# Kernel tuning notes

Hardware: AMD Instinct MI355X
Metric: run time of the kernel (lower is better)

Reference implementation:

```python
import jax, jax.numpy as jnp
import numpy as np

T, K, E, H, I = 2048, 8, 32, 1024, 768


def setup_inputs() -> dict:
    key = jax.random.key(0)
    k0, k1, k2, k3, k4, k5 = jax.random.split(key, 6)
    sh = 1.0 / np.sqrt(H).astype(np.float32)
    si = 1.0 / np.sqrt(I).astype(np.float32)
    return {
        "hidden_states": jax.random.normal(k0, (T, H), jnp.float32),
        "top_k_index": jax.random.randint(k1, (T, K), 0, E),
        "top_k_weights": jax.random.uniform(k2, (T, K), jnp.float32),
        "gate_proj": jax.random.normal(k3, (E, I, H), jnp.float32) * sh,
        "up_proj": jax.random.normal(k4, (E, I, H), jnp.float32) * sh,
        "down_proj": jax.random.normal(k5, (E, H, I), jnp.float32) * si,
    }


def reference(hidden_states, top_k_index, top_k_weights, gate_proj, up_proj, down_proj):
    # Tokens not routed to expert e get combine weight 0, so summing the
    # weighted per-expert outputs over all experts reproduces the original
    # gather -> SwiGLU MLP -> scale -> index_add_ exactly (duplicated expert
    # hits within a token's top-k sum, matching repeated index_add_).
    n_tok = hidden_states.shape[0]
    n_exp = gate_proj.shape[0]
    combine = jnp.zeros((n_tok, n_exp), hidden_states.dtype)
    combine = combine.at[jnp.arange(n_tok)[:, None], top_k_index].add(top_k_weights)

    def body(acc, xs):
        g_w, u_w, d_w, w_e = xs  # g_w,u_w: [I,H]; d_w: [H,I]; w_e: [T]
        h = jax.nn.silu(hidden_states @ g_w.T) * (hidden_states @ u_w.T)  # [T,I]
        y = h @ d_w.T  # [T,H]
        return acc + y * w_e[:, None], None

    out, _ = jax.lax.scan(
        body,
        jnp.zeros_like(hidden_states),
        (gate_proj, up_proj, down_proj, combine.T),
    )
    return out
```

## Files before the change

### kernel.cpp

```cpp
#include <hip/hip_runtime.h>

#define T_TOK 2048
#define TOPK  8
#define NEXP  32
#define HDIM  1024
#define IDIM  768
#define NPAIR (T_TOK * TOPK)
#define BM 128
#define BK 32
#define MT_MAX (NPAIR / BM + NEXP)

typedef __attribute__((ext_vector_type(8))) short short8;
typedef __attribute__((ext_vector_type(4))) float f32x4;

__device__ __forceinline__ unsigned short f2bf(float f) {
    unsigned x = __float_as_uint(f);
    unsigned r = x + 0x7fffu + ((x >> 16) & 1u);
    return (unsigned short)(r >> 16);
}
__device__ __forceinline__ float bf2f(unsigned short u) {
    return __uint_as_float(((unsigned)u) << 16);
}

__device__ __forceinline__ void gl_lds16(const unsigned short* g, void* l) {
    __builtin_amdgcn_global_load_lds((const __attribute__((address_space(1))) void*)g,
                                     (__attribute__((address_space(3))) void*)l, 16, 0, 0);
}

__device__ __forceinline__ int mt_swz(int bx) {
    return ((bx >> 4) << 4) | ((bx & 7) << 1) | ((bx >> 3) & 1);
}

#define WSYNC do { \
    asm volatile("s_waitcnt vmcnt(0)" ::: "memory"); \
    __builtin_amdgcn_s_barrier(); \
    __builtin_amdgcn_sched_barrier(0); \
} while (0)

__global__ void k_conv2(const float* __restrict__ src0, const float* __restrict__ src1,
                        unsigned short* __restrict__ dst, int n4each) {
    int i = blockIdx.x * 256 + threadIdx.x;
    const float* s = (i < n4each) ? src0 : src1;
    int j = (i < n4each) ? i : i - n4each;
    if (i < 2 * n4each) {
        float4 v = ((const float4*)s)[j];
        ushort4 o;
        o.x = f2bf(v.x); o.y = f2bf(v.y); o.z = f2bf(v.z); o.w = f2bf(v.w);
        ((ushort4*)dst)[i] = o;
    }
}

__global__ void k_conv(const float* __restrict__ src, unsigned short* __restrict__ dst, int n4) {
    int i = blockIdx.x * 256 + threadIdx.x;
    if (i < n4) {
        float4 v = ((const float4*)src)[i];
        ushort4 o;
        o.x = f2bf(v.x); o.y = f2bf(v.y); o.z = f2bf(v.z); o.w = f2bf(v.w);
        ((ushort4*)dst)[i] = o;
    }
}

__global__ void k_init(int* counts) {
    if (threadIdx.x < NEXP) counts[threadIdx.x] = 0;
}

__global__ void k_hist(const int* __restrict__ idx, int* __restrict__ counts) {
    int p = blockIdx.x * 256 + threadIdx.x;
    atomicAdd(&counts[idx[p]], 1);
}

__global__ void k_scan(const int* __restrict__ counts, int* __restrict__ offsets,
                       int* __restrict__ mtb, int* __restrict__ cursor) {
    if (threadIdx.x == 0) {
        int tot = 0, mt = 0;
        for (int e = 0; e < NEXP; ++e) {
            offsets[e] = tot; mtb[e] = mt;
            tot += counts[e];
            mt += (counts[e] + BM - 1) / BM;
        }
        offsets[NEXP] = tot; mtb[NEXP] = mt;
    }
    if (threadIdx.x < NEXP) cursor[threadIdx.x] = 0;
}

__global__ void k_scatter(const int* __restrict__ idx, int* __restrict__ cursor,
                          const int* __restrict__ offsets, int* __restrict__ pair_token,
                          int* __restrict__ pair_slot) {
    int p = blockIdx.x * 256 + threadIdx.x;
    int e = idx[p];
    int pos = atomicAdd(&cursor[e], 1);
    int slot = offsets[e] + pos;
    pair_token[slot] = p >> 3;
    pair_slot[p] = slot;
}

__global__ __launch_bounds__(256, 2) void k_gateup(
    const unsigned short* __restrict__ hid_bf, const unsigned short* __restrict__ gate_bf,
    const unsigned short* __restrict__ up_bf, const int* __restrict__ pair_token,
    const int* __restrict__ offsets, const int* __restrict__ mtb,
    unsigned short* __restrict__ h_mid)
{
    __shared__ short8 sBuf[2][1536];
    __shared__ int sInfo[4];
    int tid = threadIdx.x;
    int mt = mt_swz(blockIdx.x);
    if (tid == 0 && mt >= mtb[NEXP]) sInfo[0] = -1;
    if (tid < NEXP) {
        int lo = mtb[tid], hi = mtb[tid + 1];
        if (lo <= mt && mt < hi) {
            sInfo[0] = tid; sInfo[1] = offsets[tid];
            sInfo[2] = offsets[tid + 1] - offsets[tid];
            sInfo[3] = (mt - lo) * BM;
        }
    }
    __syncthreads();
    int e = sInfo[0];
    if (e < 0) return;
    int off = sInfo[1], Me = sInfo[2], mrow0 = sInfo[3];
    int n0 = blockIdx.y * 128;

    int wave = tid >> 6, lane = tid & 63, quad = lane >> 4, l16 = lane & 15;

    int m0 = wave * 32 + l16, m1 = m0 + 16;
    int rp0 = mrow0 + m0, rp1 = mrow0 + m1;
    int tok0 = (rp0 < Me) ? pair_token[off + rp0] : 0;
    int tok1 = (rp1 < Me) ? pair_token[off + rp1] : 0;
    const unsigned short* aG0 = hid_bf + (size_t)tok0 * HDIM + quad * 8;
    const unsigned short* aG1 = hid_bf + (size_t)tok1 * HDIM + quad * 8;
    const unsigned short* gG0 = gate_bf + ((size_t)e * IDIM + n0 + m0) * HDIM + quad * 8;
    const unsigned short* gG1 = gate_bf + ((size_t)e * IDIM + n0 + m1) * HDIM + quad * 8;
    const unsigned short* uG0 = up_bf + ((size_t)e * IDIM + n0 + m0) * HDIM + quad * 8;
    const unsigned short* uG1 = up_bf + ((size_t)e * IDIM + n0 + m1) * HDIM + quad * 8;
    const int dA = wave * 128;
    const int dG = 512 + wave * 128;
    const int dU = 1024 + wave * 128;

    int wm = (wave & 1) * 64, wn = (wave >> 1) * 64;
    int aBase = (wm >> 4) * 64 + quad * 16 + l16;
    int bBase = (wn >> 4) * 64 + quad * 16 + l16;

    f32x4 zero = {0.f, 0.f, 0.f, 0.f};
    f32x4 accg[4][4], accu[4][4];
#pragma unroll
    for (int i = 0; i < 4; ++i)
#pragma unroll
        for (int j = 0; j < 4; ++j) { accg[i][j] = zero; accu[i][j] = zero; }

#define STAGE_GU(b, k0) do { \
        short8* nb_ = &sBuf[b][0]; \
        gl_lds16(aG0 + (k0), (void*)(nb_ + dA));      gl_lds16(aG1 + (k0), (void*)(nb_ + dA + 64)); \
        gl_lds16(gG0 + (k0), (void*)(nb_ + dG));      gl_lds16(gG1 + (k0), (void*)(nb_ + dG + 64)); \
        gl_lds16(uG0 + (k0), (void*)(nb_ + dU));      gl_lds16(uG1 + (k0), (void*)(nb_ + dU + 64)); \
    } while (0)

#define COMP_GU(b) do { \
        const short8* cb_ = &sBuf[b][0]; \
        short8 af_[4]; \
        _Pragma("unroll") for (int fm = 0; fm < 4; ++fm) af_[fm] = cb_[aBase + fm * 64]; \
        _Pragma("unroll") for (int fn = 0; fn < 4; ++fn) { \
            short8 bg_ = cb_[512 + bBase + fn * 64]; \
            short8 bu_ = cb_[1024 + bBase + fn * 64]; \
            _Pragma("unroll") for (int fm = 0; fm < 4; ++fm) { \
                accg[fm][fn] = __builtin_amdgcn_mfma_f32_16x16x32_bf16(af_[fm], bg_, accg[fm][fn], 0, 0, 0); \
                accu[fm][fn] = __builtin_amdgcn_mfma_f32_16x16x32_bf16(af_[fm], bu_, accu[fm][fn], 0, 0, 0); \
            } \
        } \
    } while (0)

    STAGE_GU(0, 0);
    WSYNC;
#pragma unroll 1
    for (int it = 0; it < HDIM / BK; it += 2) {
        STAGE_GU(1, (it + 1) * BK);
        COMP_GU(0);
        WSYNC;
        if (it + 2 < HDIM / BK) STAGE_GU(0, (it + 2) * BK);
        COMP_GU(1);
        WSYNC;
    }

#pragma unroll
    for (int fm = 0; fm < 4; ++fm)
#pragma unroll
        for (int fn = 0; fn < 4; ++fn)
#pragma unroll
            for (int r = 0; r < 4; ++r) {
                int mloc = wm + fm * 16 + quad * 4 + r;
                int prow = mrow0 + mloc;
                if (prow < Me) {
                    int col = n0 + wn + fn * 16 + l16;
                    float g = accg[fm][fn][r], u = accu[fm][fn][r];
                    float h = g / (1.f + __expf(-g)) * u;
                    h_mid[(size_t)(off + prow) * IDIM + col] = f2bf(h);
                }
            }
}

__global__ __launch_bounds__(256, 2) void k_down(
    const unsigned short* __restrict__ h_mid, const unsigned short* __restrict__ down_bf,
    const int* __restrict__ offsets, const int* __restrict__ mtb,
    unsigned short* __restrict__ y_pair)
{
    __shared__ short8 sBuf[2][1536];
    __shared__ int sInfo[4];
    int tid = threadIdx.x;
    int mt = mt_swz(blockIdx.x);
    if (tid == 0 && mt >= mtb[NEXP]) sInfo[0] = -1;
    if (tid < NEXP) {
        int lo = mtb[tid], hi = mtb[tid + 1];
        if (lo <= mt && mt < hi) {
            sInfo[0] = tid; sInfo[1] = offsets[tid];
            sInfo[2] = offsets[tid + 1] - offsets[tid];
            sInfo[3] = (mt - lo) * BM;
        }
    }
    __syncthreads();
    int e = sInfo[0];
    if (e < 0) return;
    int off = sInfo[1], Me = sInfo[2], mrow0 = sInfo[3];
    int n0 = blockIdx.y * 256;

    int wave = tid >> 6, lane = tid & 63, quad = lane >> 4, l16 = lane & 15;

    int m0 = wave * 32 + l16, m1 = m0 + 16;
    int rp0 = mrow0 + m0; if (rp0 >= Me) rp0 = 0;
    int rp1 = mrow0 + m1; if (rp1 >= Me) rp1 = 0;
    const unsigned short* aG0 = h_mid + (size_t)(off + rp0) * IDIM + quad * 8;
    const unsigned short* aG1 = h_mid + (size_t)(off + rp1) * IDIM + quad * 8;
    const unsigned short* bG0 = down_bf + ((size_t)e * HDIM + n0 + wave * 64 + l16) * IDIM + quad * 8;
    const unsigned short* bG1 = bG0 + (size_t)16 * IDIM;
    const unsigned short* bG2 = bG0 + (size_t)32 * IDIM;
    const unsigned short* bG3 = bG0 + (size_t)48 * IDIM;
    const int dA = wave * 128;
    const int dB = 512 + wave * 256;

    int wm = (wave & 1) * 64, wn = (wave >> 1) * 128;
    int aBase = (wm >> 4) * 64 + quad * 16 + l16;
    int bBase = (wn >> 4) * 64 + quad * 16 + l16;

    f32x4 zero = {0.f, 0.f, 0.f, 0.f};
    f32x4 acc[4][8];
#pragma unroll
    for (int i = 0; i < 4; ++i)
#pragma unroll
        for (int j = 0; j < 8; ++j) acc[i][j] = zero;

#define STAGE_DN(b, k0) do { \
        short8* nb_ = &sBuf[b][0]; \
        gl_lds16(aG0 + (k0), (void*)(nb_ + dA));       gl_lds16(aG1 + (k0), (void*)(nb_ + dA + 64)); \
        gl_lds16(bG0 + (k0), (void*)(nb_ + dB));       gl_lds16(bG1 + (k0), (void*)(nb_ + dB + 64)); \
        gl_lds16(bG2 + (k0), (void*)(nb_ + dB + 128)); gl_lds16(bG3 + (k0), (void*)(nb_ + dB + 192)); \
    } while (0)

#define COMP_DN(b) do { \
        const short8* cb_ = &sBuf[b][0]; \
        short8 af_[4]; \
        _Pragma("unroll") for (int fm = 0; fm < 4; ++fm) af_[fm] = cb_[aBase + fm * 64]; \
        _Pragma("unroll") for (int fn = 0; fn < 8; ++fn) { \
            short8 bb_ = cb_[512 + bBase + fn * 64]; \
            _Pragma("unroll") for (int fm = 0; fm < 4; ++fm) \
                acc[fm][fn] = __builtin_amdgcn_mfma_f32_16x16x32_bf16(af_[fm], bb_, acc[fm][fn], 0, 0, 0); \
        } \
    } while (0)

    STAGE_DN(0, 0);
    WSYNC;
#pragma unroll 1
    for (int it = 0; it < IDIM / BK; it += 2) {
        STAGE_DN(1, (it + 1) * BK);
        COMP_DN(0);
        WSYNC;
        if (it + 2 < IDIM / BK) STAGE_DN(0, (it + 2) * BK);
        COMP_DN(1);
        WSYNC;
    }

#pragma unroll
    for (int fm = 0; fm < 4; ++fm)
#pragma unroll
        for (int fn = 0; fn < 8; ++fn)
#pragma unroll
            for (int r = 0; r < 4; ++r) {
                int mloc = wm + fm * 16 + quad * 4 + r;
                int prow = mrow0 + mloc;
                if (prow < Me) {
                    int col = n0 + wn + fn * 16 + l16;
                    y_pair[(size_t)(off + prow) * HDIM + col] = f2bf(acc[fm][fn][r]);
                }
            }
}

__global__ void k_reduce(const unsigned short* __restrict__ y_pair,
                         const int* __restrict__ pair_slot,
                         const float* __restrict__ topw, float* __restrict__ out)
{
    int t = blockIdx.x;
    __shared__ int ss[TOPK];
    __shared__ float sw[TOPK];
    if (threadIdx.x < TOPK) {
        ss[threadIdx.x] = pair_slot[t * TOPK + threadIdx.x];
        sw[threadIdx.x] = topw[t * TOPK + threadIdx.x];
    }
    __syncthreads();
    int c = threadIdx.x * 4;
    float a0 = 0.f, a1 = 0.f, a2 = 0.f, a3 = 0.f;
    for (int k = 0; k < TOPK; ++k) {
        const unsigned short* yr = y_pair + (size_t)ss[k] * HDIM + c;
        uint2 v = *(const uint2*)yr;
        float w = sw[k];
        a0 += w * bf2f((unsigned short)(v.x & 0xffff));
        a1 += w * bf2f((unsigned short)(v.x >> 16));
        a2 += w * bf2f((unsigned short)(v.y & 0xffff));
        a3 += w * bf2f((unsigned short)(v.y >> 16));
    }
    float4 o = {a0, a1, a2, a3};
    *(float4*)(out + (size_t)t * HDIM + c) = o;
}

extern "C" void kernel_launch(void* const* d_in, const int* in_sizes, int n_in,
                              void* d_out, int out_size, void* d_ws, size_t ws_size,
                              hipStream_t stream) {
    (void)in_sizes; (void)n_in; (void)out_size; (void)ws_size;
    const float* hidden = (const float*)d_in[0];
    const int*   tki    = (const int*)d_in[1];
    const float* tkw    = (const float*)d_in[2];
    const float* gate   = (const float*)d_in[3];
    const float* up     = (const float*)d_in[4];
    const float* down   = (const float*)d_in[5];
    float* out = (float*)d_out;

    char* w = (char*)d_ws;
    unsigned short* h_mid   = (unsigned short*)w;
    unsigned short* hid_bf  = (unsigned short*)(w + 25165824);
    unsigned short* gate_bf = (unsigned short*)(w + 29360128);
    unsigned short* up_bf   = (unsigned short*)(w + 79691776);
    unsigned short* down_bf = gate_bf;
    unsigned short* y_pair  = up_bf;
    int* ib = (int*)(w + 130023424);
    int* pair_token = ib;
    int* pair_slot  = ib + NPAIR;
    int* counts     = ib + 2 * NPAIR;
    int* cursor     = counts + NEXP;
    int* offsets    = cursor + NEXP;
    int* mtb        = offsets + NEXP + 1;

    const int W4 = NEXP * IDIM * HDIM / 4;
    const int H4 = T_TOK * HDIM / 4;

    k_init<<<1, 64, 0, stream>>>(counts);
    k_hist<<<NPAIR / 256, 256, 0, stream>>>(tki, counts);
    k_scan<<<1, 64, 0, stream>>>(counts, offsets, mtb, cursor);
    k_scatter<<<NPAIR / 256, 256, 0, stream>>>(tki, cursor, offsets, pair_token, pair_slot);

    k_conv<<<(H4 + 255) / 256, 256, 0, stream>>>(hidden, hid_bf, H4);
    k_conv2<<<(2 * W4 + 255) / 256, 256, 0, stream>>>(gate, up, gate_bf, W4);

    k_gateup<<<dim3(MT_MAX, IDIM / 128), 256, 0, stream>>>(hid_bf, gate_bf, up_bf,
                                                           pair_token, offsets, mtb, h_mid);

    k_conv<<<(W4 + 255) / 256, 256, 0, stream>>>(down, down_bf, W4);

    k_down<<<dim3(MT_MAX, HDIM / 256), 256, 0, stream>>>(h_mid, down_bf, offsets, mtb, y_pair);
    k_reduce<<<T_TOK, 256, 0, stream>>>(y_pair, pair_slot, tkw, out);
}
```

Before: 560.8 us.

## Keep two K-tiles in flight with partial vmcnt waits in MoE GEMMs

Restructures the double-buffered K loops of the gate/up and down GEMM kernels so that two stages of global-to-LDS loads are issued ahead. Each compute step now waits only on the older stage via vmcnt(6) instead of draining all outstanding loads, with barriers around each compute. The aim is to hide global load latency behind MFMA work rather than stalling on every tile. The risk is that the vmcnt(6) count must exactly match the number of loads per stage, and dropping the sched_barrier lets the compiler reorder around the LDS reads.

```diff
diff --git a/kernel.cpp b/kernel.cpp
--- a/kernel.cpp
+++ b/kernel.cpp
@@ -31,11 +31,8 @@
     return ((bx >> 4) << 4) | ((bx & 7) << 1) | ((bx >> 3) & 1);
 }
 
-#define WSYNC do { \
-    asm volatile("s_waitcnt vmcnt(0)" ::: "memory"); \
-    __builtin_amdgcn_s_barrier(); \
-    __builtin_amdgcn_sched_barrier(0); \
-} while (0)
+#define VMCNT(n) asm volatile("s_waitcnt vmcnt(" #n ")" ::: "memory")
+#define BARRIER  __builtin_amdgcn_s_barrier()
 
 __global__ void k_conv2(const float* __restrict__ src0, const float* __restrict__ src1,
                         unsigned short* __restrict__ dst, int n4each) {
@@ -168,16 +165,14 @@
     } while (0)
 
     STAGE_GU(0, 0);
-    WSYNC;
+    STAGE_GU(1, BK);
 #pragma unroll 1
-    for (int it = 0; it < HDIM / BK; it += 2) {
-        STAGE_GU(1, (it + 1) * BK);
-        COMP_GU(0);
-        WSYNC;
-        if (it + 2 < HDIM / BK) STAGE_GU(0, (it + 2) * BK);
-        COMP_GU(1);
-        WSYNC;
-    }
+    for (int tt = 0; tt < HDIM / BK - 2; tt += 2) {
+        VMCNT(6); BARRIER; COMP_GU(0); BARRIER; STAGE_GU(0, (tt + 2) * BK);
+        VMCNT(6); BARRIER; COMP_GU(1); BARRIER; STAGE_GU(1, (tt + 3) * BK);
+    }
+    VMCNT(6); BARRIER; COMP_GU(0);
+    VMCNT(0); BARRIER; COMP_GU(1);
 
 #pragma unroll
     for (int fm = 0; fm < 4; ++fm)
@@ -264,16 +259,14 @@
     } while (0)
 
     STAGE_DN(0, 0);
-    WSYNC;
+    STAGE_DN(1, BK);
 #pragma unroll 1
-    for (int it = 0; it < IDIM / BK; it += 2) {
-        STAGE_DN(1, (it + 1) * BK);
-        COMP_DN(0);
-        WSYNC;
-        if (it + 2 < IDIM / BK) STAGE_DN(0, (it + 2) * BK);
-        COMP_DN(1);
-        WSYNC;
-    }
+    for (int tt = 0; tt < IDIM / BK - 2; tt += 2) {
+        VMCNT(6); BARRIER; COMP_DN(0); BARRIER; STAGE_DN(0, (tt + 2) * BK);
+        VMCNT(6); BARRIER; COMP_DN(1); BARRIER; STAGE_DN(1, (tt + 3) * BK);
+    }
+    VMCNT(6); BARRIER; COMP_DN(0);
+    VMCNT(0); BARRIER; COMP_DN(1);
 
 #pragma unroll
     for (int fm = 0; fm < 4; ++fm)
```

Measured after the change: 545.5 us. -2.7%, faster.

## Fuse fp32-to-bf16 weight conversion into grouped GEMM load pipeline

Applied to the files above, without the earlier changes.

Drops the separate conversion kernels for the gate, up and down weights. The GEMM kernels now load the fp32 weights straight into registers, convert them to bf16 and write them to LDS, while activations still arrive through direct global-to-LDS loads. The pipeline is rebuilt with explicit vmcnt/lgkmcnt waits so the register prefetch of the next tile overlaps with MFMA compute. This removes a full pass that wrote and re-read about 150MB of weights. In exchange each weight tile is read as fp32 (twice the bytes) and reloaded by every token tile of an expert, with conversion and more VGPR pressure on the critical path.

```diff
diff --git a/kernel.cpp b/kernel.cpp
--- a/kernel.cpp
+++ b/kernel.cpp
@@ -22,6 +22,15 @@
     return __uint_as_float(((unsigned)u) << 16);
 }
 
+__device__ __forceinline__ short8 pack8(float4 a, float4 b) {
+    short8 r;
+    r[0] = (short)f2bf(a.x); r[1] = (short)f2bf(a.y);
+    r[2] = (short)f2bf(a.z); r[3] = (short)f2bf(a.w);
+    r[4] = (short)f2bf(b.x); r[5] = (short)f2bf(b.y);
+    r[6] = (short)f2bf(b.z); r[7] = (short)f2bf(b.w);
+    return r;
+}
+
 __device__ __forceinline__ void gl_lds16(const unsigned short* g, void* l) {
     __builtin_amdgcn_global_load_lds((const __attribute__((address_space(1))) void*)g,
                                      (__attribute__((address_space(3))) void*)l, 16, 0, 0);
@@ -31,24 +40,10 @@
     return ((bx >> 4) << 4) | ((bx & 7) << 1) | ((bx >> 3) & 1);
 }
 
-#define WSYNC do { \
-    asm volatile("s_waitcnt vmcnt(0)" ::: "memory"); \
-    __builtin_amdgcn_s_barrier(); \
-    __builtin_amdgcn_sched_barrier(0); \
-} while (0)
-
-__global__ void k_conv2(const float* __restrict__ src0, const float* __restrict__ src1,
-                        unsigned short* __restrict__ dst, int n4each) {
-    int i = blockIdx.x * 256 + threadIdx.x;
-    const float* s = (i < n4each) ? src0 : src1;
-    int j = (i < n4each) ? i : i - n4each;
-    if (i < 2 * n4each) {
-        float4 v = ((const float4*)s)[j];
-        ushort4 o;
-        o.x = f2bf(v.x); o.y = f2bf(v.y); o.z = f2bf(v.z); o.w = f2bf(v.w);
-        ((ushort4*)dst)[i] = o;
-    }
-}
+#define VMCNT(n)  asm volatile("s_waitcnt vmcnt(" #n ")" ::: "memory")
+#define LGKM0     asm volatile("s_waitcnt lgkmcnt(0)" ::: "memory")
+#define MEMFENCE  asm volatile("" ::: "memory")
+#define BARRIER   __builtin_amdgcn_s_barrier()
 
 __global__ void k_conv(const float* __restrict__ src, unsigned short* __restrict__ dst, int n4) {
     int i = blockIdx.x * 256 + threadIdx.x;
@@ -95,8 +90,8 @@
 }
 
 __global__ __launch_bounds__(256, 2) void k_gateup(
-    const unsigned short* __restrict__ hid_bf, const unsigned short* __restrict__ gate_bf,
-    const unsigned short* __restrict__ up_bf, const int* __restrict__ pair_token,
+    const unsigned short* __restrict__ hid_bf, const float* __restrict__ gateF,
+    const float* __restrict__ upF, const int* __restrict__ pair_token,
     const int* __restrict__ offsets, const int* __restrict__ mtb,
     unsigned short* __restrict__ h_mid)
 {
@@ -127,13 +122,14 @@
     int tok1 = (rp1 < Me) ? pair_token[off + rp1] : 0;
     const unsigned short* aG0 = hid_bf + (size_t)tok0 * HDIM + quad * 8;
     const unsigned short* aG1 = hid_bf + (size_t)tok1 * HDIM + quad * 8;
-    const unsigned short* gG0 = gate_bf + ((size_t)e * IDIM + n0 + m0) * HDIM + quad * 8;
-    const unsigned short* gG1 = gate_bf + ((size_t)e * IDIM + n0 + m1) * HDIM + quad * 8;
-    const unsigned short* uG0 = up_bf + ((size_t)e * IDIM + n0 + m0) * HDIM + quad * 8;
-    const unsigned short* uG1 = up_bf + ((size_t)e * IDIM + n0 + m1) * HDIM + quad * 8;
     const int dA = wave * 128;
-    const int dG = 512 + wave * 128;
-    const int dU = 1024 + wave * 128;
+
+    const float* gF0 = gateF + ((size_t)e * IDIM + n0 + m0) * HDIM + quad * 8;
+    const float* gF1 = gateF + ((size_t)e * IDIM + n0 + m1) * HDIM + quad * 8;
+    const float* uF0 = upF   + ((size_t)e * IDIM + n0 + m0) * HDIM + quad * 8;
+    const float* uF1 = upF   + ((size_t)e * IDIM + n0 + m1) * HDIM + quad * 8;
+    const int wslot0 = wave * 128 + quad * 16 + l16;
+    const int wslot1 = wslot0 + 64;
 
     int wm = (wave & 1) * 64, wn = (wave >> 1) * 64;
     int aBase = (wm >> 4) * 64 + quad * 16 + l16;
@@ -146,11 +142,25 @@
 #pragma unroll
         for (int j = 0; j < 4; ++j) { accg[i][j] = zero; accu[i][j] = zero; }
 
-#define STAGE_GU(b, k0) do { \
-        short8* nb_ = &sBuf[b][0]; \
-        gl_lds16(aG0 + (k0), (void*)(nb_ + dA));      gl_lds16(aG1 + (k0), (void*)(nb_ + dA + 64)); \
-        gl_lds16(gG0 + (k0), (void*)(nb_ + dG));      gl_lds16(gG1 + (k0), (void*)(nb_ + dG + 64)); \
-        gl_lds16(uG0 + (k0), (void*)(nb_ + dU));      gl_lds16(uG1 + (k0), (void*)(nb_ + dU + 64)); \
+    float4 vg0a, vg0b, vg1a, vg1b, vu0a, vu0b, vu1a, vu1b;
+
+#define ADMA_GU(b, kk) do { \
+        gl_lds16(aG0 + (kk), (void*)(&sBuf[b][dA])); \
+        gl_lds16(aG1 + (kk), (void*)(&sBuf[b][dA + 64])); \
+    } while (0)
+
+#define BLOAD_GU(kk) do { \
+        vg0a = *(const float4*)(gF0 + (kk)); vg0b = *(const float4*)(gF0 + (kk) + 4); \
+        vg1a = *(const float4*)(gF1 + (kk)); vg1b = *(const float4*)(gF1 + (kk) + 4); \
+        vu0a = *(const float4*)(uF0 + (kk)); vu0b = *(const float4*)(uF0 + (kk) + 4); \
+        vu1a = *(const float4*)(uF1 + (kk)); vu1b = *(const float4*)(uF1 + (kk) + 4); \
+    } while (0)
+
+#define CVTWR_GU(b) do { \
+        sBuf[b][512  + wslot0] = pack8(vg0a, vg0b); \
+        sBuf[b][512  + wslot1] = pack8(vg1a, vg1b); \
+        sBuf[b][1024 + wslot0] = pack8(vu0a, vu0b); \
+        sBuf[b][1024 + wslot1] = pack8(vu1a, vu1b); \
     } while (0)
 
 #define COMP_GU(b) do { \
@@ -167,17 +177,35 @@
         } \
     } while (0)
 
-    STAGE_GU(0, 0);
-    WSYNC;
+    BLOAD_GU(0);
+    VMCNT(0);
+    CVTWR_GU(0);
+    ADMA_GU(0, 0);
+    MEMFENCE;
+    BLOAD_GU(BK);
+
 #pragma unroll 1
-    for (int it = 0; it < HDIM / BK; it += 2) {
-        STAGE_GU(1, (it + 1) * BK);
+    for (int tt = 0; tt <= HDIM / BK - 4; tt += 2) {
+        VMCNT(8); LGKM0; BARRIER;
+        ADMA_GU(1, (tt + 1) * BK);
+        VMCNT(2);
+        CVTWR_GU(1);
+        BLOAD_GU((tt + 2) * BK);
         COMP_GU(0);
-        WSYNC;
-        if (it + 2 < HDIM / BK) STAGE_GU(0, (it + 2) * BK);
+        VMCNT(8); LGKM0; BARRIER;
+        ADMA_GU(0, (tt + 2) * BK);
+        VMCNT(2);
+        CVTWR_GU(0);
+        BLOAD_GU((tt + 3) * BK);
         COMP_GU(1);
-        WSYNC;
-    }
+    }
+    VMCNT(8); LGKM0; BARRIER;
+    ADMA_GU(1, (HDIM / BK - 1) * BK);
+    VMCNT(2);
+    CVTWR_GU(1);
+    COMP_GU(0);
+    VMCNT(0); LGKM0; BARRIER;
+    COMP_GU(1);
 
 #pragma unroll
     for (int fm = 0; fm < 4; ++fm)
@@ -197,7 +225,7 @@
 }
 
 __global__ __launch_bounds__(256, 2) void k_down(
-    const unsigned short* __restrict__ h_mid, const unsigned short* __restrict__ down_bf,
+    const unsigned short* __restrict__ h_mid, const float* __restrict__ downF,
     const int* __restrict__ offsets, const int* __restrict__ mtb,
     unsigned short* __restrict__ y_pair)
 {
@@ -227,12 +255,13 @@
     int rp1 = mrow0 + m1; if (rp1 >= Me) rp1 = 0;
     const unsigned short* aG0 = h_mid + (size_t)(off + rp0) * IDIM + quad * 8;
     const unsigned short* aG1 = h_mid + (size_t)(off + rp1) * IDIM + quad * 8;
-    const unsigned short* bG0 = down_bf + ((size_t)e * HDIM + n0 + wave * 64 + l16) * IDIM + quad * 8;
-    const unsigned short* bG1 = bG0 + (size_t)16 * IDIM;
-    const unsigned short* bG2 = bG0 + (size_t)32 * IDIM;
-    const unsigned short* bG3 = bG0 + (size_t)48 * IDIM;
     const int dA = wave * 128;
-    const int dB = 512 + wave * 256;
+
+    const float* dF0 = downF + ((size_t)e * HDIM + n0 + wave * 64 + l16) * IDIM + quad * 8;
+    const float* dF1 = dF0 + (size_t)16 * IDIM;
+    const float* dF2 = dF0 + (size_t)32 * IDIM;
+    const float* dF3 = dF0 + (size_t)48 * IDIM;
+    const int wslot0 = wave * 256 + quad * 16 + l16;
 
     int wm = (wave & 1) * 64, wn = (wave >> 1) * 128;
     int aBase = (wm >> 4) * 64 + quad * 16 + l16;
@@ -245,11 +274,25 @@
 #pragma unroll
         for (int j = 0; j < 8; ++j) acc[i][j] = zero;
 
-#define STAGE_DN(b, k0) do { \
-        short8* nb_ = &sBuf[b][0]; \
-        gl_lds16(aG0 + (k0), (void*)(nb_ + dA));       gl_lds16(aG1 + (k0), (void*)(nb_ + dA + 64)); \
-        gl_lds16(bG0 + (k0), (void*)(nb_ + dB));       gl_lds16(bG1 + (k0), (void*)(nb_ + dB + 64)); \
-        gl_lds16(bG2 + (k0), (void*)(nb_ + dB + 128)); gl_lds16(bG3 + (k0), (void*)(nb_ + dB + 192)); \
+    float4 v0a, v0b, v1a, v1b, v2a, v2b, v3a, v3b;
+
+#define ADMA_DN(b, kk) do { \
+        gl_lds16(aG0 + (kk), (void*)(&sBuf[b][dA])); \
+        gl_lds16(aG1 + (kk), (void*)(&sBuf[b][dA + 64])); \
+    } while (0)
+
+#define BLOAD_DN(kk) do { \
+        v0a = *(const float4*)(dF0 + (kk)); v0b = *(const float4*)(dF0 + (kk) + 4); \
+        v1a = *(const float4*)(dF1 + (kk)); v1b = *(const float4*)(dF1 + (kk) + 4); \
+        v2a = *(const float4*)(dF2 + (kk)); v2b = *(const float4*)(dF2 + (kk) + 4); \
+        v3a = *(const float4*)(dF3 + (kk)); v3b = *(const float4*)(dF3 + (kk) + 4); \
+    } while (0)
+
+#define CVTWR_DN(b) do { \
+        sBuf[b][512 + wslot0]       = pack8(v0a, v0b); \
+        sBuf[b][512 + wslot0 + 64]  = pack8(v1a, v1b); \
+        sBuf[b][512 + wslot0 + 128] = pack8(v2a, v2b); \
+        sBuf[b][512 + wslot0 + 192] = pack8(v3a, v3b); \
     } while (0)
 
 #define COMP_DN(b) do { \
@@ -263,17 +306,35 @@
         } \
     } while (0)
 
-    STAGE_DN(0, 0);
-    WSYNC;
+    BLOAD_DN(0);
+    VMCNT(0);
+    CVTWR_DN(0);
+    ADMA_DN(0, 0);
+    MEMFENCE;
+    BLOAD_DN(BK);
+
 #pragma unroll 1
-    for (int it = 0; it < IDIM / BK; it += 2) {
-        STAGE_DN(1, (it + 1) * BK);
+    for (int tt = 0; tt <= IDIM / BK - 4; tt += 2) {
+        VMCNT(8); LGKM0; BARRIER;
+        ADMA_DN(1, (tt + 1) * BK);
+        VMCNT(2);
+        CVTWR_DN(1);
+        BLOAD_DN((tt + 2) * BK);
         COMP_DN(0);
-        WSYNC;
-        if (it + 2 < IDIM / BK) STAGE_DN(0, (it + 2) * BK);
+        VMCNT(8); LGKM0; BARRIER;
+        ADMA_DN(0, (tt + 2) * BK);
+        VMCNT(2);
+        CVTWR_DN(0);
+        BLOAD_DN((tt + 3) * BK);
         COMP_DN(1);
-        WSYNC;
-    }
+    }
+    VMCNT(8); LGKM0; BARRIER;
+    ADMA_DN(1, (IDIM / BK - 1) * BK);
+    VMCNT(2);
+    CVTWR_DN(1);
+    COMP_DN(0);
+    VMCNT(0); LGKM0; BARRIER;
+    COMP_DN(1);
 
 #pragma unroll
     for (int fm = 0; fm < 4; ++fm)
@@ -332,10 +393,7 @@
     char* w = (char*)d_ws;
     unsigned short* h_mid   = (unsigned short*)w;
     unsigned short* hid_bf  = (unsigned short*)(w + 25165824);
-    unsigned short* gate_bf = (unsigned short*)(w + 29360128);
-    unsigned short* up_bf   = (unsigned short*)(w + 79691776);
-    unsigned short* down_bf = gate_bf;
-    unsigned short* y_pair  = up_bf;
+    unsigned short* y_pair  = (unsigned short*)(w + 29360128);
     int* ib = (int*)(w + 130023424);
     int* pair_token = ib;
     int* pair_slot  = ib + NPAIR;
@@ -344,7 +402,6 @@
     int* offsets    = cursor + NEXP;
     int* mtb        = offsets + NEXP + 1;
 
-    const int W4 = NEXP * IDIM * HDIM / 4;
     const int H4 = T_TOK * HDIM / 4;
 
     k_init<<<1, 64, 0, stream>>>(counts);
@@ -353,13 +410,10 @@
     k_scatter<<<NPAIR / 256, 256, 0, stream>>>(tki, cursor, offsets, pair_token, pair_slot);
 
     k_conv<<<(H4 + 255) / 256, 256, 0, stream>>>(hidden, hid_bf, H4);
-    k_conv2<<<(2 * W4 + 255) / 256, 256, 0, stream>>>(gate, up, gate_bf, W4);
-
-    k_gateup<<<dim3(MT_MAX, IDIM / 128), 256, 0, stream>>>(hid_bf, gate_bf, up_bf,
+
+    k_gateup<<<dim3(MT_MAX, IDIM / 128), 256, 0, stream>>>(hid_bf, gate, up,
                                                            pair_token, offsets, mtb, h_mid);
 
-    k_conv<<<(W4 + 255) / 256, 256, 0, stream>>>(down, down_bf, W4);
-
-    k_down<<<dim3(MT_MAX, HDIM / 256), 256, 0, stream>>>(h_mid, down_bf, offsets, mtb, y_pair);
+    k_down<<<dim3(MT_MAX, HDIM / 256), 256, 0, stream>>>(h_mid, down, offsets, mtb, y_pair);
     k_reduce<<<T_TOK, 256, 0, stream>>>(y_pair, pair_slot, tkw, out);
 }
```

Result: slower. 611.4 us (+9.0%).
